# Kernel optimization log

Measured on AMD Instinct MI355X. Metric: run time of the kernel, lower is better.

## Reference

```python
import jax, jax.numpy as jnp
import numpy as np

HIDDEN = 1024
HEADS = 16
HEAD_DIM = HIDDEN // HEADS


def setup_inputs() -> dict:
    key = jax.random.key(0)
    ks = jax.random.split(key, 5)
    B, T = 4, 2048
    x = jax.random.normal(ks[0], (B, T, HIDDEN), dtype=jnp.float32)
    s = 1.0 / np.sqrt(HIDDEN)
    qkv_w = jax.random.normal(ks[1], (HIDDEN, 3 * HIDDEN), dtype=jnp.float32) * s
    qkv_b = jnp.zeros((3 * HIDDEN,), dtype=jnp.float32)
    proj_w = jax.random.normal(ks[2], (HIDDEN, HIDDEN), dtype=jnp.float32) * s
    proj_b = jnp.zeros((HIDDEN,), dtype=jnp.float32)
    return {"x": x, "qkv_w": qkv_w, "qkv_b": qkv_b, "proj_w": proj_w, "proj_b": proj_b}


def reference(x, qkv_w, qkv_b, proj_w, proj_b):
    B, T, C = x.shape
    qkv = x @ qkv_w + qkv_b                       # [B,T,3C]
    qkv = qkv.reshape(B, T, 3, HEADS, HEAD_DIM)
    q, k, v = qkv[:, :, 0], qkv[:, :, 1], qkv[:, :, 2]  # [B,T,H,D]
    scale = HEAD_DIM ** -0.5
    scores = jnp.einsum('bthd,bshd->bhts', q, k) * scale  # [B,H,T,T]
    attn = jax.nn.softmax(scores, axis=-1)
    out = jnp.einsum('bhts,bshd->bthd', attn, v).reshape(B, T, C)
    return out @ proj_w + proj_b
```

## Files before the change

### kernel.cpp

```cpp
#include <hip/hip_runtime.h>
#include <hip/hip_bf16.h>

#define HID  1024
#define N3   3072
#define NH   16
#define HD   64
#define SEQ  2048
#define NB   4
#define MTOT 8192

typedef unsigned short u16x8 __attribute__((ext_vector_type(8)));
typedef unsigned short u16x4 __attribute__((ext_vector_type(4)));
typedef float f32x4 __attribute__((ext_vector_type(4)));

static __device__ __forceinline__ unsigned short f2bf(float f) {
    union { float f; unsigned u; } v; v.f = f;
    unsigned r = (v.u + 0x7fffu + ((v.u >> 16) & 1u)) >> 16;
    return (unsigned short)r;
}

static __device__ __forceinline__ float fexp2(float x) {
    float r; asm("v_exp_f32 %0, %1" : "=v"(r) : "v"(x)); return r;
}

typedef __attribute__((address_space(3))) void* lds_vp;
typedef const __attribute__((address_space(1))) void* gbl_vp;

static __device__ __forceinline__ void gload16(const void* g, void* l) {
    __builtin_amdgcn_global_load_lds((gbl_vp)g, (lds_vp)l, 16, 0, 0);
}

#define CQ 0.18033688011112042f

__global__ void k_cvt(const float* __restrict__ in, unsigned short* __restrict__ out, int n) {
    int i = (blockIdx.x * 256 + threadIdx.x) * 8;
    if (i >= n) return;
    float4 a = *(const float4*)(in + i);
    float4 b = *(const float4*)(in + i + 4);
    u16x8 p;
    p[0]=f2bf(a.x); p[1]=f2bf(a.y); p[2]=f2bf(a.z); p[3]=f2bf(a.w);
    p[4]=f2bf(b.x); p[5]=f2bf(b.y); p[6]=f2bf(b.z); p[7]=f2bf(b.w);
    *(u16x8*)(out + i) = p;
}

__global__ void k_tcvt(const float* __restrict__ W, unsigned short* __restrict__ WT, int R, int C) {
    int tiles_c = C >> 6;
    int k0 = (blockIdx.x / tiles_c) << 6;
    int n0 = (blockIdx.x % tiles_c) << 6;
    __shared__ unsigned short tile[64 * 64];
    int tid = threadIdx.x;
    #pragma unroll
    for (int it = 0; it < 2; ++it) {
        int task = it * 256 + tid;
        int t = task >> 3, dc = task & 7;
        const float* src = W + (size_t)(k0 + t) * C + n0 + dc * 8;
        float4 a = *(const float4*)src;
        float4 b = *(const float4*)(src + 4);
        u16x8 p;
        p[0]=f2bf(a.x); p[1]=f2bf(a.y); p[2]=f2bf(a.z); p[3]=f2bf(a.w);
        p[4]=f2bf(b.x); p[5]=f2bf(b.y); p[6]=f2bf(b.z); p[7]=f2bf(b.w);
        *(u16x8*)&tile[t * 64 + ((dc ^ (t & 7)) << 3)] = p;
    }
    __syncthreads();
    #pragma unroll
    for (int it = 0; it < 2; ++it) {
        int task = it * 256 + tid;
        int d = task >> 3, tc = task & 7;
        u16x8 p;
        #pragma unroll
        for (int i = 0; i < 8; ++i) {
            int ii = (i + tc) & 7;
            int t = tc * 8 + ii;
            p[ii] = tile[t * 64 + ((((d >> 3) ^ (t & 7)) << 3)) + (d & 7)];
        }
        *(u16x8*)(WT + (size_t)(n0 + d) * R + k0 + tc * 8) = p;
    }
}

__global__ void k_tv(const unsigned short* __restrict__ qkv, unsigned short* __restrict__ vT) {
    int bh = blockIdx.x >> 5;
    int t0 = (blockIdx.x & 31) << 6;
    int b = bh >> 4, h = bh & 15;
    __shared__ unsigned short tile[64 * 64];
    int tid = threadIdx.x;
    #pragma unroll
    for (int it = 0; it < 2; ++it) {
        int task = it * 256 + tid;
        int t = task >> 3, dc = task & 7;
        const unsigned short* src = qkv + (size_t)(b * SEQ + t0 + t) * N3 + 2048 + h * 64 + dc * 8;
        *(u16x8*)&tile[t * 64 + ((dc ^ (t & 7)) << 3)] = *(const u16x8*)src;
    }
    __syncthreads();
    #pragma unroll
    for (int it = 0; it < 2; ++it) {
        int task = it * 256 + tid;
        int d = task >> 3, tc = task & 7;
        u16x8 p;
        #pragma unroll
        for (int i = 0; i < 8; ++i) {
            int ii = (i + tc) & 7;
            int t = tc * 8 + ii;
            p[ii] = tile[t * 64 + ((((d >> 3) ^ (t & 7)) << 3)) + (d & 7)];
        }
        *(u16x8*)(vT + (size_t)(bh * 64 + d) * SEQ + t0 + tc * 8) = p;
    }
}

template<int BF16OUT, int QSCALE>
__global__ __launch_bounds__(256) void k_gemm(const unsigned short* __restrict__ A,
                                              const unsigned short* __restrict__ BT,
                                              const float* __restrict__ bias,
                                              void* __restrict__ Cout, int M, int N, int K) {
    int tiles_n = N >> 7;
    int bm = blockIdx.x / tiles_n, bn = blockIdx.x % tiles_n;
    int tid = threadIdx.x, wid = tid >> 6, lane = tid & 63;
    int wr = wid >> 1, wc = wid & 1;
    int fr = lane & 15, fg = lane >> 4;

    __shared__ unsigned short lA[128 * 64];
    __shared__ unsigned short lB[128 * 64];

    f32x4 acc[4][4];
    #pragma unroll
    for (int m = 0; m < 4; ++m)
        #pragma unroll
        for (int n = 0; n < 4; ++n)
            acc[m][n] = (f32x4){0.f, 0.f, 0.f, 0.f};

    int srow = lane >> 3;
    int sch  = (lane & 7) ^ srow;
    const unsigned short* aSrc[4]; const unsigned short* bSrc[4];
    unsigned short* aDst[4]; unsigned short* bDst[4];
    #pragma unroll
    for (int i = 0; i < 4; ++i) {
        int rbase = i * 32 + wid * 8;
        aSrc[i] = A  + (size_t)(bm * 128 + rbase + srow) * K + sch * 8;
        bSrc[i] = BT + (size_t)(bn * 128 + rbase + srow) * K + sch * 8;
        aDst[i] = lA + rbase * 64;
        bDst[i] = lB + rbase * 64;
    }

    for (int k0 = 0; k0 < K; k0 += 64) {
        __syncthreads();
        #pragma unroll
        for (int i = 0; i < 4; ++i) {
            gload16(aSrc[i] + k0, aDst[i]);
            gload16(bSrc[i] + k0, bDst[i]);
        }
        asm volatile("s_waitcnt vmcnt(0)" ::: "memory");
        __syncthreads();
        #pragma unroll
        for (int kk = 0; kk < 2; ++kk) {
            u16x8 af[4], bf[4];
            #pragma unroll
            for (int m = 0; m < 4; ++m) {
                int row = wr * 64 + m * 16 + fr;
                int ch = ((kk << 2) + fg) ^ (fr & 7);
                af[m] = *(const u16x8*)&lA[row * 64 + ch * 8];
            }
            #pragma unroll
            for (int n = 0; n < 4; ++n) {
                int row = wc * 64 + n * 16 + fr;
                int ch = ((kk << 2) + fg) ^ (fr & 7);
                bf[n] = *(const u16x8*)&lB[row * 64 + ch * 8];
            }
            #pragma unroll
            for (int m = 0; m < 4; ++m)
                #pragma unroll
                for (int n = 0; n < 4; ++n)
                    acc[m][n] = __builtin_amdgcn_mfma_f32_16x16x32_bf16(af[m], bf[n], acc[m][n], 0, 0, 0);
        }
    }

    #pragma unroll
    for (int n = 0; n < 4; ++n) {
        int col = bn * 128 + wc * 64 + n * 16 + fr;
        float bv = bias[col];
        float cs = (QSCALE && col < 1024) ? CQ : 1.0f;
        #pragma unroll
        for (int m = 0; m < 4; ++m) {
            int row0 = bm * 128 + wr * 64 + m * 16 + fg * 4;
            #pragma unroll
            for (int r = 0; r < 4; ++r) {
                float v = (acc[m][n][r] + bv) * cs;
                if (BF16OUT)
                    ((unsigned short*)Cout)[(size_t)(row0 + r) * N + col] = f2bf(v);
                else
                    ((float*)Cout)[(size_t)(row0 + r) * N + col] = v;
            }
        }
    }
}

__global__ __launch_bounds__(256) void k_attn(const unsigned short* __restrict__ qkv,
                                              const unsigned short* __restrict__ vT,
                                              unsigned short* __restrict__ out) {
    int bh = blockIdx.x >> 4;
    int q0 = (blockIdx.x & 15) << 7;
    int b = bh >> 4, h = bh & 15;
    int tid = threadIdx.x, wid = tid >> 6, lane = tid & 63;
    int fr = lane & 15, fg = lane >> 4;

    __shared__ unsigned short lK[128 * 64];
    __shared__ unsigned short lV[64 * 128];
    const char* lKb = (const char*)lK;
    const char* lVb = (const char*)lV;

    int srow = lane >> 3;
    int sch  = (lane & 7) ^ srow;

    u16x8 ones;
    #pragma unroll
    for (int i = 0; i < 8; ++i) ones[i] = 0x3F80;

    int kfb[2], vbb[4];
    #pragma unroll
    for (int kk = 0; kk < 2; ++kk) kfb[kk] = fr * 128 + (((((kk << 2) + fg) ^ (fr & 7))) << 4);
    #pragma unroll
    for (int kk = 0; kk < 4; ++kk) vbb[kk] = fr * 256 + (((((kk << 2) + fg) ^ (fr & 7))) << 4);

    const unsigned short* qbase = qkv + (size_t)(b * SEQ) * N3 + h * 64;
    #pragma unroll
    for (int i = 0; i < 4; ++i) {
        int rbase = i * 32 + wid * 8;
        gload16(qbase + (size_t)(q0 + rbase + srow) * N3 + sch * 8, lK + rbase * 64);
    }
    asm volatile("s_waitcnt vmcnt(0)" ::: "memory");
    __syncthreads();
    u16x8 qf[2][2];
    #pragma unroll
    for (int j = 0; j < 2; ++j)
        #pragma unroll
        for (int kk = 0; kk < 2; ++kk)
            qf[j][kk] = *(const u16x8*)(lKb + kfb[kk] + (wid * 32 + j * 16) * 128);

    f32x4 o[2][4];
    #pragma unroll
    for (int j = 0; j < 2; ++j)
        #pragma unroll
        for (int i = 0; i < 4; ++i)
            o[j][i] = (f32x4){0.f, 0.f, 0.f, 0.f};
    f32x4 o_sum[2];
    o_sum[0] = (f32x4){0.f, 0.f, 0.f, 0.f};
    o_sum[1] = (f32x4){0.f, 0.f, 0.f, 0.f};

    const unsigned short* kp[4]; const unsigned short* vp[4];
    unsigned short* kDst[4]; unsigned short* vDst[4];
    {
        const unsigned short* kbase = qkv + (size_t)(b * SEQ) * N3 + HID + h * 64;
        const unsigned short* vbase = vT + (size_t)(bh * 64) * SEQ;
        #pragma unroll
        for (int i = 0; i < 4; ++i) {
            int rbase = i * 32 + wid * 8;
            kp[i] = kbase + (size_t)(rbase + srow) * N3 + sch * 8;
            kDst[i] = lK + rbase * 64;
            int vrow = i * 16 + wid * 4 + (lane >> 4);
            int vch = (lane & 15) ^ (vrow & 7);
            vp[i] = vbase + (size_t)vrow * SEQ + vch * 8;
            vDst[i] = lV + (i * 16 + wid * 4) * 128;
        }
    }

    for (int s0 = 0; s0 < SEQ; s0 += 128) {
        __syncthreads();
        #pragma unroll
        for (int i = 0; i < 4; ++i) {
            gload16(kp[i], kDst[i]);  kp[i] += 128 * N3;
            gload16(vp[i], vDst[i]);  vp[i] += 128;
        }
        asm volatile("s_waitcnt vmcnt(0)" ::: "memory");
        __syncthreads();

        u16x8 pb[2][4];
        #pragma unroll
        for (int ih = 0; ih < 2; ++ih) {
            f32x4 sa[2][4];
            #pragma unroll
            for (int j = 0; j < 2; ++j)
                #pragma unroll
                for (int il = 0; il < 4; ++il)
                    sa[j][il] = (f32x4){0.f, 0.f, 0.f, 0.f};
            #pragma unroll
            for (int kk = 0; kk < 2; ++kk) {
                u16x8 kf[4];
                #pragma unroll
                for (int il = 0; il < 4; ++il)
                    kf[il] = *(const u16x8*)(lKb + kfb[kk] + (ih * 4 + il) * 2048);
                #pragma unroll
                for (int j = 0; j < 2; ++j)
                    #pragma unroll
                    for (int il = 0; il < 4; ++il)
                        sa[j][il] = __builtin_amdgcn_mfma_f32_16x16x32_bf16(kf[il], qf[j][kk], sa[j][il], 0, 0, 0);
            }

            #pragma unroll
            for (int j = 0; j < 2; ++j) {
                unsigned pk[2][2][2];
                #pragma unroll
                for (int il = 0; il < 4; ++il) {
                    #pragma unroll
                    for (int p = 0; p < 2; ++p) {
                        float ea = fexp2(sa[j][il][2 * p]);
                        float eb = fexp2(sa[j][il][2 * p + 1]);
                        unsigned rr;
                        asm("v_cvt_pk_bf16_f32 %0, %1, %2" : "=v"(rr) : "v"(ea), "v"(eb));
                        pk[il >> 1][il & 1][p] = rr;
                    }
                }
                #pragma unroll
                for (int t2 = 0; t2 < 2; ++t2) {
                    #pragma unroll
                    for (int p = 0; p < 2; ++p) {
                        asm("v_permlane32_swap_b32 %0, %1" : "+v"(pk[t2][0][p]), "+v"(pk[t2][1][p]));
                        asm("v_permlane16_swap_b32 %0, %1" : "+v"(pk[t2][0][p]), "+v"(pk[t2][1][p]));
                    }
                    union { unsigned u[4]; u16x8 v; } w;
                    w.u[0] = pk[t2][0][0]; w.u[1] = pk[t2][0][1];
                    w.u[2] = pk[t2][1][0]; w.u[3] = pk[t2][1][1];
                    pb[j][ih * 2 + t2] = w.v;
                    o_sum[j] = __builtin_amdgcn_mfma_f32_16x16x32_bf16(ones, pb[j][ih * 2 + t2], o_sum[j], 0, 0, 0);
                }
            }
        }

        #pragma unroll
        for (int kk = 0; kk < 4; ++kk) {
            u16x8 vb[4];
            #pragma unroll
            for (int i = 0; i < 4; ++i)
                vb[i] = *(const u16x8*)(lVb + vbb[kk] + i * 4096);
            #pragma unroll
            for (int j = 0; j < 2; ++j)
                #pragma unroll
                for (int i = 0; i < 4; ++i)
                    o[j][i] = __builtin_amdgcn_mfma_f32_16x16x32_bf16(vb[i], pb[j][kk], o[j][i], 0, 0, 0);
        }
    }

    #pragma unroll
    for (int j = 0; j < 2; ++j) {
        float inv = 1.f / o_sum[j][0];
        size_t t = q0 + wid * 32 + j * 16 + fr;
        #pragma unroll
        for (int i = 0; i < 4; ++i) {
            u16x4 st;
            st[0] = f2bf(o[j][i][0] * inv);
            st[1] = f2bf(o[j][i][1] * inv);
            st[2] = f2bf(o[j][i][2] * inv);
            st[3] = f2bf(o[j][i][3] * inv);
            *(u16x4*)&out[(size_t)(b * SEQ + t) * HID + h * 64 + i * 16 + fg * 4] = st;
        }
    }
}

extern "C" void kernel_launch(void* const* d_in, const int* in_sizes, int n_in,
                              void* d_out, int out_size, void* d_ws, size_t ws_size,
                              hipStream_t stream) {
    const float* x      = (const float*)d_in[0];
    const float* qkv_w  = (const float*)d_in[1];
    const float* qkv_b  = (const float*)d_in[2];
    const float* proj_w = (const float*)d_in[3];
    const float* proj_b = (const float*)d_in[4];
    float* out = (float*)d_out;

    char* ws = (char*)d_ws;
    unsigned short* xb     = (unsigned short*)ws;
    unsigned short* vTb    = (unsigned short*)ws;
    unsigned short* wqkvT  = (unsigned short*)(ws + 16777216);
    unsigned short* wprojT = (unsigned short*)(ws + 23068672);
    unsigned short* qkvb   = (unsigned short*)(ws + 25165824);
    unsigned short* aob    = (unsigned short*)(ws + 75497472);

    k_cvt<<<4096, 256, 0, stream>>>(x, xb, MTOT * HID);
    k_tcvt<<<768, 256, 0, stream>>>(qkv_w, wqkvT, HID, N3);
    k_tcvt<<<256, 256, 0, stream>>>(proj_w, wprojT, HID, HID);
    k_gemm<1, 1><<<1536, 256, 0, stream>>>(xb, wqkvT, qkv_b, (void*)qkvb, MTOT, N3, HID);
    k_tv<<<2048, 256, 0, stream>>>(qkvb, vTb);
    k_attn<<<1024, 256, 0, stream>>>(qkvb, vTb, aob);
    k_gemm<0, 0><<<512, 256, 0, stream>>>(aob, wprojT, proj_b, (void*)out, MTOT, HID, HID);
}
```

Measured before the change: 214.3 us.

## Double-buffer K/V tiles in attention and swizzle block order for locality

The attention kernel now keeps two LDS buffers for K and V and issues the global-to-LDS loads for the next key block before computing on the current one. It waits with a partial vmcnt so those loads overlap the MFMA and exp work. Both the GEMM and attention kernels remap blockIdx with a stride-8 interleave, which changes which tiles run together and likely targets cache or XCD locality. The cost is double the LDS per block, which may reduce occupancy, plus an extra barrier per iteration.

```diff
diff --git a/kernel.cpp b/kernel.cpp
--- a/kernel.cpp
+++ b/kernel.cpp
@@ -112,7 +112,8 @@
                                               const float* __restrict__ bias,
                                               void* __restrict__ Cout, int M, int N, int K) {
     int tiles_n = N >> 7;
-    int bm = blockIdx.x / tiles_n, bn = blockIdx.x % tiles_n;
+    int bid = (blockIdx.x & 7) * (gridDim.x >> 3) + (blockIdx.x >> 3);
+    int bm = bid / tiles_n, bn = bid % tiles_n;
     int tid = threadIdx.x, wid = tid >> 6, lane = tid & 63;
     int wr = wid >> 1, wc = wid & 1;
     int fr = lane & 15, fg = lane >> 4;
@@ -195,19 +196,21 @@
 __global__ __launch_bounds__(256) void k_attn(const unsigned short* __restrict__ qkv,
                                               const unsigned short* __restrict__ vT,
                                               unsigned short* __restrict__ out) {
-    int bh = blockIdx.x >> 4;
-    int q0 = (blockIdx.x & 15) << 7;
+    int bid = (blockIdx.x & 7) * 128 + (blockIdx.x >> 3);
+    int bh = bid >> 4;
+    int q0 = (bid & 15) << 7;
     int b = bh >> 4, h = bh & 15;
     int tid = threadIdx.x, wid = tid >> 6, lane = tid & 63;
     int fr = lane & 15, fg = lane >> 4;
 
-    __shared__ unsigned short lK[128 * 64];
-    __shared__ unsigned short lV[64 * 128];
+    __shared__ unsigned short lK[2][128 * 64];
+    __shared__ unsigned short lV[2][64 * 128];
     const char* lKb = (const char*)lK;
     const char* lVb = (const char*)lV;
 
     int srow = lane >> 3;
     int sch  = (lane & 7) ^ srow;
+    int woff = wid * 512;
 
     u16x8 ones;
     #pragma unroll
@@ -223,9 +226,8 @@
     #pragma unroll
     for (int i = 0; i < 4; ++i) {
         int rbase = i * 32 + wid * 8;
-        gload16(qbase + (size_t)(q0 + rbase + srow) * N3 + sch * 8, lK + rbase * 64);
-    }
-    asm volatile("s_waitcnt vmcnt(0)" ::: "memory");
+        gload16(qbase + (size_t)(q0 + rbase + srow) * N3 + sch * 8, (unsigned short*)lK + rbase * 64);
+    }
     __syncthreads();
     u16x8 qf[2][2];
     #pragma unroll
@@ -233,6 +235,7 @@
         #pragma unroll
         for (int kk = 0; kk < 2; ++kk)
             qf[j][kk] = *(const u16x8*)(lKb + kfb[kk] + (wid * 32 + j * 16) * 128);
+    __syncthreads();
 
     f32x4 o[2][4];
     #pragma unroll
@@ -245,31 +248,41 @@
     o_sum[1] = (f32x4){0.f, 0.f, 0.f, 0.f};
 
     const unsigned short* kp[4]; const unsigned short* vp[4];
-    unsigned short* kDst[4]; unsigned short* vDst[4];
     {
         const unsigned short* kbase = qkv + (size_t)(b * SEQ) * N3 + HID + h * 64;
         const unsigned short* vbase = vT + (size_t)(bh * 64) * SEQ;
         #pragma unroll
         for (int i = 0; i < 4; ++i) {
-            int rbase = i * 32 + wid * 8;
-            kp[i] = kbase + (size_t)(rbase + srow) * N3 + sch * 8;
-            kDst[i] = lK + rbase * 64;
+            kp[i] = kbase + (size_t)(i * 32 + wid * 8 + srow) * N3 + sch * 8;
             int vrow = i * 16 + wid * 4 + (lane >> 4);
             int vch = (lane & 15) ^ (vrow & 7);
             vp[i] = vbase + (size_t)vrow * SEQ + vch * 8;
-            vDst[i] = lV + (i * 16 + wid * 4) * 128;
-        }
-    }
-
-    for (int s0 = 0; s0 < SEQ; s0 += 128) {
-        __syncthreads();
-        #pragma unroll
-        for (int i = 0; i < 4; ++i) {
-            gload16(kp[i], kDst[i]);  kp[i] += 128 * N3;
-            gload16(vp[i], vDst[i]);  vp[i] += 128;
-        }
-        asm volatile("s_waitcnt vmcnt(0)" ::: "memory");
-        __syncthreads();
+        }
+    }
+
+#define STAGE(bufi) do {                                                   \
+        unsigned short* kd = (unsigned short*)lK + (bufi) * 8192 + woff;   \
+        unsigned short* vd = (unsigned short*)lV + (bufi) * 8192 + woff;   \
+        _Pragma("unroll")                                                  \
+        for (int i = 0; i < 4; ++i) {                                      \
+            gload16(kp[i], kd + i * 2048);  kp[i] += 128 * N3;             \
+            gload16(vp[i], vd + i * 2048);  vp[i] += 128;                  \
+        }                                                                  \
+    } while (0)
+
+    STAGE(0);
+
+    for (int t = 0; t < 16; ++t) {
+        int cur = t & 1;
+        int cb = cur * 16384;
+        if (t < 15) {
+            STAGE(cur ^ 1);
+            asm volatile("s_waitcnt vmcnt(8)" ::: "memory");
+        } else {
+            asm volatile("s_waitcnt vmcnt(0)" ::: "memory");
+        }
+        __builtin_amdgcn_s_barrier();
+        __builtin_amdgcn_sched_barrier(0);
 
         u16x8 pb[2][4];
         #pragma unroll
@@ -285,7 +298,7 @@
                 u16x8 kf[4];
                 #pragma unroll
                 for (int il = 0; il < 4; ++il)
-                    kf[il] = *(const u16x8*)(lKb + kfb[kk] + (ih * 4 + il) * 2048);
+                    kf[il] = *(const u16x8*)(lKb + cb + kfb[kk] + (ih * 4 + il) * 2048);
                 #pragma unroll
                 for (int j = 0; j < 2; ++j)
                     #pragma unroll
@@ -328,14 +341,17 @@
             u16x8 vb[4];
             #pragma unroll
             for (int i = 0; i < 4; ++i)
-                vb[i] = *(const u16x8*)(lVb + vbb[kk] + i * 4096);
+                vb[i] = *(const u16x8*)(lVb + cb + vbb[kk] + i * 4096);
             #pragma unroll
             for (int j = 0; j < 2; ++j)
                 #pragma unroll
                 for (int i = 0; i < 4; ++i)
                     o[j][i] = __builtin_amdgcn_mfma_f32_16x16x32_bf16(vb[i], pb[j][kk], o[j][i], 0, 0, 0);
         }
-    }
+
+        __syncthreads();
+    }
+#undef STAGE
 
     #pragma unroll
     for (int j = 0; j < 2; ++j) {
```

New measurement: 204.9 us. -4.4%, faster.
